# Kernel tuning notes

Hardware: AMD Instinct MI355X
Metric: run time of the kernel (lower is better)

## Reference

```python
import math
import jax, jax.numpy as jnp
import numpy as np

B, V, F, H, W = 1, 2, 4, 16, 28
TPF = H * W            # 448 tokens per frame
VS = F * TPF           # 1792 tokens per view
TS = V * VS            # 3584 total tokens
DIM, NH = 1536, 12
HD = DIM // NH         # 128
EPS = 1e-6
SCALE = 1.0 / math.sqrt(HD)


def _rope_angle_table(max_len=1024):
    # Wan-style 3D rope: head_dim//2 = 64 channels split [22, 21, 21] for (f, h, w)
    parts = []
    for full in (44, 42, 42):
        inv = 1.0 / (10000.0 ** (np.arange(0, full, 2) / full))
        parts.append(np.outer(np.arange(max_len), inv))
    return np.concatenate(parts, axis=1).astype(np.float32)  # [max_len, 64]


def setup_inputs():
    key = jax.random.key(0)
    ks = jax.random.split(key, 6)
    p = lambda k, shp: 0.02 * jax.random.normal(k, shp, dtype=jnp.float32)
    return {
        "x": jax.random.normal(ks[0], (B, TS, DIM), dtype=jnp.float32),
        "freqs": jnp.asarray(_rope_angle_table()),
        "q_w": p(ks[1], (DIM, DIM)), "q_b": jnp.zeros((DIM,), jnp.float32),
        "k_w": p(ks[2], (DIM, DIM)), "k_b": jnp.zeros((DIM,), jnp.float32),
        "v_w": p(ks[3], (DIM, DIM)), "v_b": jnp.zeros((DIM,), jnp.float32),
        "o_w": p(ks[4], (DIM, DIM)), "o_b": jnp.zeros((DIM,), jnp.float32),
        "norm_q_w": jnp.ones((DIM,), jnp.float32),
        "norm_k_w": jnp.ones((DIM,), jnp.float32),
        "seq_lens": jnp.full((B,), TS, jnp.int32),
        "view_grid_sizes": jnp.broadcast_to(jnp.array([F, H, W], jnp.int32), (B, V, 3)),
        "view_seq_lens": jnp.full((B, V), VS, jnp.int32),
        "total_seq_lens": jnp.full((B,), TS, jnp.int32),
    }


def _rms_norm(x, w):
    x32 = x.astype(jnp.float32)
    y = x32 * jax.lax.rsqrt(jnp.mean(x32 * x32, axis=-1, keepdims=True) + EPS)
    return y.astype(x.dtype) * w


def _rope_angles(freqs):
    c = HD // 2                                   # 64
    s0, s1 = c - 2 * (c // 3), c // 3             # 22, 21
    af = jnp.broadcast_to(freqs[:F, None, None, :s0], (F, H, W, s0))
    ah = jnp.broadcast_to(freqs[None, :H, None, s0:s0 + s1], (F, H, W, s1))
    aw = jnp.broadcast_to(freqs[None, None, :W, s0 + s1:c], (F, H, W, c - s0 - s1))
    return jnp.concatenate([af, ah, aw], axis=-1).reshape(VS, c)  # [VS, 64]


def _apply_rope(x, ang):
    # x: [N, S, NH, HD]; pairs are (x[..., 2i], x[..., 2i+1]) as in view_as_complex
    cos = jnp.cos(ang)[None, :, None, :]
    sin = jnp.sin(ang)[None, :, None, :]
    xr = x.reshape(x.shape[:-1] + (HD // 2, 2))
    r0 = xr[..., 0] * cos - xr[..., 1] * sin
    r1 = xr[..., 0] * sin + xr[..., 1] * cos
    return jnp.stack([r0, r1], axis=-1).reshape(x.shape)


def _attn_lse(q, k, v):
    # q,k,v: [N, S, NH, HD] -> out [N, S, NH, HD], lse [N, S, NH]
    logits = jnp.einsum('bqhd,bkhd->bhqk', q, k) * SCALE
    lse = jax.nn.logsumexp(logits, axis=-1)       # [N, NH, Sq]
    p = jnp.exp(logits - lse[..., None])
    out = jnp.einsum('bhqk,bkhd->bqhd', p, v)
    return out, jnp.transpose(lse, (0, 2, 1))


def _forward(x, freqs, q_w, q_b, k_w, k_b, v_w, v_b, o_w, o_b, norm_q_w, norm_k_w):
    xv = x[:, :TS]
    q = _rms_norm(xv @ q_w.T + q_b, norm_q_w)
    k = _rms_norm(xv @ k_w.T + k_b, norm_k_w)
    v = xv @ v_w.T + v_b
    q = q.reshape(B * V, VS, NH, HD)
    k = k.reshape(B * V, VS, NH, HD)
    v = v.reshape(B * V, VS, NH, HD)
    ang = _rope_angles(freqs)
    q = _apply_rope(q, ang)
    k = _apply_rope(k, ang)
    # intra-view attention over the full view sequence
    out_i, lse_i = _attn_lse(q, k, v)
    # cross-view per-frame attention: swap the two views for K/V
    k_sw = k.reshape(B, V, F, TPF, NH, HD)[:, ::-1].reshape(B * V * F, TPF, NH, HD)
    v_sw = v.reshape(B, V, F, TPF, NH, HD)[:, ::-1].reshape(B * V * F, TPF, NH, HD)
    q_c = q.reshape(B * V * F, TPF, NH, HD)
    out_c, lse_c = _attn_lse(q_c, k_sw, v_sw)
    out_i = out_i.reshape(B, V, F, TPF, NH, HD)
    lse_i = lse_i.reshape(B, V, F, TPF, NH)
    out_c = out_c.reshape(B, V, F, TPF, NH, HD)
    lse_c = lse_c.reshape(B, V, F, TPF, NH)
    # online-softmax-style LSE merge of the two attention results
    lse_u = jnp.logaddexp(lse_i, lse_c)
    fused = (jnp.exp(lse_i - lse_u)[..., None] * out_i
             + jnp.exp(lse_c - lse_u)[..., None] * out_c)
    fused = fused.reshape(B, TS, DIM)
    return fused @ o_w.T + o_b


def reference(x, freqs, q_w, q_b, k_w, k_b, v_w, v_b, o_w, o_b, norm_q_w, norm_k_w,
              seq_lens, view_grid_sizes, view_seq_lens, total_seq_lens):
    del seq_lens, view_grid_sizes, view_seq_lens, total_seq_lens  # validated layout constants
    return _forward(x, freqs, q_w, q_b, k_w, k_b, v_w, v_b, o_w, o_b, norm_q_w, norm_k_w)
```

## Files before the change

kernel.cpp:

```cpp
#include <hip/hip_runtime.h>

#define TS 3584
#define VS 1792
#define TPF 448
#define NHEAD 12
#define HDIM 128
#define DMODEL 1536
#define QK_PRESCALE (0.08838834764831845f * 1.4426950408889634f)

typedef unsigned short u16;
typedef unsigned int u32;
typedef __attribute__((ext_vector_type(8))) short bf16x8;
typedef __attribute__((ext_vector_type(4))) float f32x4;

__device__ __forceinline__ float u2f(u32 u) { union { u32 u; float f; } c; c.u = u; return c.f; }
__device__ __forceinline__ float blo(u32 u) { return u2f(u << 16); }
__device__ __forceinline__ float bhi(u32 u) { return u2f(u & 0xffff0000u); }
__device__ __forceinline__ u16 f2b(float f) {
  union { float f; u32 u; } c; c.f = f;
  return (u16)((c.u + 0x7fffu + ((c.u >> 16) & 1u)) >> 16);
}

__device__ __forceinline__ float exp2fast(float x) {
#if __has_builtin(__builtin_amdgcn_exp2f)
  return __builtin_amdgcn_exp2f(x);
#else
  float r; asm("v_exp_f32 %0, %1" : "=v"(r) : "v"(x)); return r;
#endif
}

__device__ __forceinline__ void gl16(const u16* g, u16* l) {
  __builtin_amdgcn_global_load_lds(
      (const __attribute__((address_space(1))) void*)g,
      (__attribute__((address_space(3))) void*)l, 16, 0, 0);
}

__global__ __launch_bounds__(256) void convert_bf16(
    const float* __restrict__ x, const float* __restrict__ qw,
    const float* __restrict__ kw, const float* __restrict__ vw,
    const float* __restrict__ ow, u16* __restrict__ xb,
    u16* __restrict__ wqkv, u16* __restrict__ owb) {
  const int z = blockIdx.y;
  const float* src;
  u16* dst;
  int n8;
  if (z == 0)      { src = x;  dst = xb;  n8 = TS * DMODEL / 8; }
  else if (z == 4) { src = ow; dst = owb; n8 = DMODEL * DMODEL / 8; }
  else {
    src = (z == 1) ? qw : (z == 2) ? kw : vw;
    dst = wqkv + (size_t)(z - 1) * DMODEL * DMODEL;
    n8 = DMODEL * DMODEL / 8;
  }
  const int idx = blockIdx.x * 256 + threadIdx.x;
  if (idx >= n8) return;
  const float4 a = ((const float4*)src)[2 * idx];
  const float4 b = ((const float4*)src)[2 * idx + 1];
  uint4 o;
  o.x = (u32)f2b(a.x) | ((u32)f2b(a.y) << 16);
  o.y = (u32)f2b(a.z) | ((u32)f2b(a.w) << 16);
  o.z = (u32)f2b(b.x) | ((u32)f2b(b.y) << 16);
  o.w = (u32)f2b(b.z) | ((u32)f2b(b.w) << 16);
  ((uint4*)dst)[idx] = o;
}

template <bool QKV>
__global__ __launch_bounds__(256) void gemm_mfma(
    const u16* __restrict__ A, const u16* __restrict__ W,
    const float* __restrict__ b0, const float* __restrict__ b1,
    const float* __restrict__ b2,
    u16* __restrict__ o0, u16* __restrict__ o1, u16* __restrict__ o2,
    float* __restrict__ of) {
  __shared__ __align__(16) u16 Als[128 * 64];
  __shared__ __align__(16) u16 Bls[128 * 64];
  const int t = threadIdx.x;
  const int wave = t >> 6, lane = t & 63, col = lane & 15, quad = lane >> 4;
  const int nwg = gridDim.x * gridDim.y;
  const int dlin = blockIdx.y * gridDim.x + blockIdx.x;
  const int wk = (dlin & 7) * (nwg >> 3) + (dlin >> 3);
  const int by = wk / gridDim.x, bx = wk - by * gridDim.x;
  const int m0 = by * 128, n0 = bx * 128;
  const int wm = (wave & 1) * 64, wn = (wave >> 1) * 64;

  const int srow = lane >> 3;
  const int sch = (lane & 7) ^ srow;
  const u16* pA[4];
  const u16* pB[4];
#pragma unroll
  for (int i = 0; i < 4; ++i) {
    const int r = i * 32 + wave * 8 + srow;
    pA[i] = A + (size_t)(m0 + r) * DMODEL + sch * 8;
    pB[i] = W + (size_t)(n0 + r) * DMODEL + sch * 8;
  }

  f32x4 acc[4][4];
#pragma unroll
  for (int i = 0; i < 4; ++i)
#pragma unroll
    for (int j = 0; j < 4; ++j) acc[i][j] = (f32x4){0.f, 0.f, 0.f, 0.f};

  for (int k0 = 0; k0 < DMODEL; k0 += 64) {
    __syncthreads();
#pragma unroll
    for (int i = 0; i < 4; ++i) {
      gl16(pA[i] + k0, &Als[i * 2048 + wave * 512]);
      gl16(pB[i] + k0, &Bls[i * 2048 + wave * 512]);
    }
    __syncthreads();
#pragma unroll
    for (int s = 0; s < 2; ++s) {
      bf16x8 af[4], bv[4];
#pragma unroll
      for (int i = 0; i < 4; ++i) {
        const int r = wm + i * 16 + col;
        af[i] = *(const bf16x8*)&Als[r * 64 + (((s * 4 + quad) ^ (r & 7)) * 8)];
      }
#pragma unroll
      for (int j = 0; j < 4; ++j) {
        const int r = wn + j * 16 + col;
        bv[j] = *(const bf16x8*)&Bls[r * 64 + (((s * 4 + quad) ^ (r & 7)) * 8)];
      }
#pragma unroll
      for (int i = 0; i < 4; ++i)
#pragma unroll
        for (int j = 0; j < 4; ++j)
          acc[i][j] = __builtin_amdgcn_mfma_f32_16x16x32_bf16(af[i], bv[j], acc[i][j], 0, 0, 0);
    }
  }

#pragma unroll
  for (int j = 0; j < 4; ++j) {
    const int ng = n0 + wn + j * 16 + col;
    if constexpr (QKV) {
      const int sec = ng / DMODEL;
      const int nn = ng - sec * DMODEL;
      u16* dst = sec == 0 ? o0 : (sec == 1 ? o1 : o2);
      const float bias = sec == 0 ? b0[nn] : (sec == 1 ? b1[nn] : b2[nn]);
#pragma unroll
      for (int i = 0; i < 4; ++i) {
        const int mb = m0 + wm + i * 16 + quad * 4;
#pragma unroll
        for (int r = 0; r < 4; ++r)
          dst[(size_t)(mb + r) * DMODEL + nn] = f2b(acc[i][j][r] + bias);
      }
    } else {
      const float bias = b0[ng];
#pragma unroll
      for (int i = 0; i < 4; ++i) {
        const int mb = m0 + wm + i * 16 + quad * 4;
#pragma unroll
        for (int r = 0; r < 4; ++r)
          of[(size_t)(mb + r) * DMODEL + ng] = acc[i][j][r] + bias;
      }
    }
  }
}

__global__ __launch_bounds__(256) void rmsnorm_rope(
    u16* qbuf, u16* kbuf, const float* __restrict__ freqs,
    const float* __restrict__ nqw, const float* __restrict__ nkw) {
  const int tok = blockIdx.x;
  u32* row = (u32*)((blockIdx.y == 0 ? qbuf : kbuf) + (size_t)tok * DMODEL);
  const float* w = blockIdx.y == 0 ? nqw : nkw;
  const int t = threadIdx.x;
  const u32 u0 = row[t], u1 = row[t + 256], u2 = row[t + 512];
  float px[3] = { blo(u0), blo(u1), blo(u2) };
  float py[3] = { bhi(u0), bhi(u1), bhi(u2) };
  float ss = px[0] * px[0] + py[0] * py[0] + px[1] * px[1] + py[1] * py[1] +
             px[2] * px[2] + py[2] * py[2];
#pragma unroll
  for (int off = 32; off; off >>= 1) ss += __shfl_xor(ss, off);
  __shared__ float red[4];
  if ((t & 63) == 0) red[t >> 6] = ss;
  __syncthreads();
  float rstd = rsqrtf((red[0] + red[1] + red[2] + red[3]) * (1.0f / DMODEL) + 1e-6f);
  if (blockIdx.y == 0) rstd *= QK_PRESCALE;
  const int p = tok % VS;
  const int fi = p / TPF, rem = p % TPF, hi = rem / 28, wi = rem % 28;
#pragma unroll
  for (int jj = 0; jj < 3; ++jj) {
    const int pj = t + jj * 256;
    const int i = pj & 63;
    const int prow = (i < 22) ? fi : ((i < 43) ? hi : wi);
    const float ang = freqs[prow * 64 + i];
    float sn, cs;
    sincosf(ang, &sn, &cs);
    const float a = px[jj] * rstd * w[2 * pj], b = py[jj] * rstd * w[2 * pj + 1];
    row[pj] = (u32)f2b(a * cs - b * sn) | ((u32)f2b(a * sn + b * cs) << 16);
  }
}

__global__ __launch_bounds__(128) void transpose_v(
    const u16* __restrict__ v, u16* __restrict__ vt) {
  __shared__ __align__(16) u16 T[128 * 128];
  const int h = blockIdx.y;
  const int t0 = blockIdx.x * 128;
  const int t = threadIdx.x;
#pragma unroll
  for (int i = 0; i < 16; ++i) {
    int idx = t + i * 128;
    int tok = idx >> 4, hd8 = idx & 15;
    *(uint4*)&T[tok * 128 + ((hd8 ^ (tok & 7)) * 8)] =
        *(const uint4*)(v + (size_t)(t0 + tok) * DMODEL + h * HDIM + hd8 * 8);
  }
  __syncthreads();
  const int hb = t >> 3;
#pragma unroll
  for (int half = 0; half < 2; ++half) {
    const int tb = (t & 7) + half * 8;
    uint4 M[8];
#pragma unroll
    for (int r = 0; r < 8; ++r)
      M[r] = *(const uint4*)&T[(tb * 8 + r) * 128 + ((hb ^ r) * 8)];
    uint4 O[8];
#pragma unroll
    for (int c2 = 0; c2 < 4; ++c2) {
      const u32* A = (const u32*)&M[2 * c2];
      const u32* Bp = (const u32*)&M[2 * c2 + 1];
#pragma unroll
      for (int jh = 0; jh < 4; ++jh) {
        u32 a = A[jh], b = Bp[jh];
        ((u32*)&O[2 * jh])[c2] = (a & 0xffffu) | (b << 16);
        ((u32*)&O[2 * jh + 1])[c2] = (a >> 16) | (b & 0xffff0000u);
      }
    }
#pragma unroll
    for (int j = 0; j < 8; ++j)
      *(uint4*)(vt + (size_t)(h * HDIM + hb * 8 + j) * TS + t0 + tb * 8) = O[j];
  }
}

__global__ __launch_bounds__(256) void attn_mfma(
    const u16* __restrict__ q, const u16* __restrict__ k,
    const u16* __restrict__ vt, u16* __restrict__ fused) {
  __shared__ __align__(16) u16 Kls[2 * 32 * 128];
  __shared__ __align__(16) u16 Vls[2 * 128 * 32];
  const int t = threadIdx.x;
  const int wave = t >> 6, lane = t & 63;
  const int col = lane & 15, quad = lane >> 4;
  const int d = blockIdx.y * 56 + blockIdx.x;
  const int wk = (d & 7) * 84 + (d >> 3);
  const int h = wk / 56;
  const int qb = wk - h * 56;
  const int q0 = qb * 64;
  const int vview = q0 / VS;
  const int fidx = (q0 % VS) / TPF;
  const int base0 = vview * VS;
  const int base1 = (1 - vview) * VS + fidx * TPF;
  const int jmpd = base1 - base0 - 1760;

  bf16x8 qfrag[4];
#pragma unroll
  for (int c = 0; c < 4; ++c)
    qfrag[c] = *(const bf16x8*)(q + (size_t)(q0 + wave * 16 + col) * DMODEL +
                                h * HDIM + ((c * 4 + quad) << 3));

  const u16* ksrc[2];
  const u16* vsrc[2];
#pragma unroll
  for (int j = 0; j < 2; ++j) {
    const int ci = (wave * 2 + j) * 64 + lane;
    const int key = ci >> 4, c = ci & 15;
    const int k4 = ((key >> 1) & 12) | (key & 3);
    ksrc[j] = k + (size_t)(base0 + key) * DMODEL + h * HDIM + ((c ^ k4) << 3);
    const int hd = ci >> 2, sl = ci & 3;
    vsrc[j] = vt + (size_t)(h * HDIM + hd) * TS + base0 + ((sl ^ (hd & 3)) << 3);
  }
  const int r0 = ((col & 12) << 1) | (col & 3);
  int koffu[4];
#pragma unroll
  for (int c = 0; c < 4; ++c) koffu[c] = r0 * 128 + (((c * 4 + quad) ^ col) << 3);
  const int voffu = col * 32 + ((quad ^ (col & 3)) << 3);

#pragma unroll
  for (int j = 0; j < 2; ++j) {
    gl16(ksrc[j], &Kls[(wave * 2 + j) * 512]);
    gl16(vsrc[j], &Vls[(wave * 2 + j) * 512]);
  }
  int ts = 1;
#pragma unroll
  for (int j = 0; j < 2; ++j) { ksrc[j] += 32 * DMODEL; vsrc[j] += 32; }

  f32x4 accO[8];
#pragma unroll
  for (int c = 0; c < 8; ++c) accO[c] = (f32x4){0.f, 0.f, 0.f, 0.f};
  float m_run = -1e30f, l_run = 0.f;

#define AITER(CUR, LAST)                                                       \
  do {                                                                         \
    if (!(LAST)) {                                                             \
      _Pragma("unroll") for (int j = 0; j < 2; ++j) {                          \
        gl16(ksrc[j], &Kls[((CUR) ^ 1) * 4096 + (wave * 2 + j) * 512]);        \
        gl16(vsrc[j], &Vls[((CUR) ^ 1) * 4096 + (wave * 2 + j) * 512]);        \
      }                                                                        \
      const int dd = (ts == 55) ? jmpd : 32; ++ts;                             \
      _Pragma("unroll") for (int j = 0; j < 2; ++j) {                          \
        ksrc[j] += (ptrdiff_t)dd * DMODEL; vsrc[j] += dd;                      \
      }                                                                        \
    }                                                                          \
    asm volatile("s_waitcnt vmcnt(%0)" ::"i"((LAST) ? 0 : 4) : "memory");      \
    __builtin_amdgcn_s_barrier();                                              \
    asm volatile("" ::: "memory");                                             \
    f32x4 s0 = (f32x4){0.f, 0.f, 0.f, 0.f}, s1 = s0;                           \
    __builtin_amdgcn_s_setprio(1);                                             \
    _Pragma("unroll") for (int c = 0; c < 4; ++c) {                            \
      bf16x8 ka0 = *(const bf16x8*)&Kls[(CUR) * 4096 + koffu[c]];              \
      bf16x8 ka1 = *(const bf16x8*)&Kls[(CUR) * 4096 + koffu[c] + 512];        \
      s0 = __builtin_amdgcn_mfma_f32_16x16x32_bf16(ka0, qfrag[c], s0, 0, 0, 0);\
      s1 = __builtin_amdgcn_mfma_f32_16x16x32_bf16(ka1, qfrag[c], s1, 0, 0, 0);\
    }                                                                          \
    __builtin_amdgcn_s_setprio(0);                                             \
    float lmax = fmaxf(fmaxf(fmaxf(s0[0], s0[1]), fmaxf(s0[2], s0[3])),        \
                       fmaxf(fmaxf(s1[0], s1[1]), fmaxf(s1[2], s1[3])));       \
    lmax = fmaxf(lmax, __shfl_xor(lmax, 16));                                  \
    lmax = fmaxf(lmax, __shfl_xor(lmax, 32));                                  \
    if (__any(lmax > m_run + 8.f)) {                                           \
      const float mnew = fmaxf(m_run, lmax);                                   \
      const float alpha = exp2fast(m_run - mnew);                              \
      _Pragma("unroll") for (int c = 0; c < 8; ++c) {                          \
        accO[c][0] *= alpha; accO[c][1] *= alpha;                              \
        accO[c][2] *= alpha; accO[c][3] *= alpha;                              \
      }                                                                        \
      l_run *= alpha;                                                          \
      m_run = mnew;                                                            \
    }                                                                          \
    float ps = 0.f;                                                            \
    _Pragma("unroll") for (int r = 0; r < 4; ++r) {                            \
      s0[r] = exp2fast(s0[r] - m_run); s1[r] = exp2fast(s1[r] - m_run);        \
      ps += s0[r] + s1[r];                                                     \
    }                                                                          \
    union { u32 w[4]; bf16x8 v; } pu;                                          \
    asm("v_cvt_pk_bf16_f32 %0, %1, %2" : "=v"(pu.w[0]) : "v"(s0[0]), "v"(s0[1])); \
    asm("v_cvt_pk_bf16_f32 %0, %1, %2" : "=v"(pu.w[1]) : "v"(s0[2]), "v"(s0[3])); \
    asm("v_cvt_pk_bf16_f32 %0, %1, %2" : "=v"(pu.w[2]) : "v"(s1[0]), "v"(s1[1])); \
    asm("v_cvt_pk_bf16_f32 %0, %1, %2" : "=v"(pu.w[3]) : "v"(s1[2]), "v"(s1[3])); \
    __builtin_amdgcn_s_setprio(1);                                             \
    _Pragma("unroll") for (int c = 0; c < 8; ++c) {                            \
      bf16x8 va = *(const bf16x8*)&Vls[(CUR) * 4096 + voffu + c * 512];        \
      accO[c] = __builtin_amdgcn_mfma_f32_16x16x32_bf16(va, pu.v, accO[c], 0, 0, 0); \
    }                                                                          \
    __builtin_amdgcn_s_setprio(0);                                             \
    if (!(LAST)) {                                                             \
      asm volatile("" ::: "memory");                                           \
      __builtin_amdgcn_s_barrier();                                            \
      asm volatile("" ::: "memory");                                           \
    }                                                                          \
    ps += __shfl_xor(ps, 16);                                                  \
    ps += __shfl_xor(ps, 32);                                                  \
    l_run += ps;                                                               \
  } while (0)

  for (int tt = 0; tt < 34; ++tt) {
    AITER(0, false);
    AITER(1, false);
  }
  AITER(0, false);
  AITER(1, true);
#undef AITER

  const float inv = 1.0f / l_run;
  const int token = q0 + wave * 16 + col;
  u16* orow = fused + (size_t)token * DMODEL + h * HDIM;
#pragma unroll
  for (int c = 0; c < 8; ++c) {
    uint2 ov;
    ov.x = (u32)f2b(accO[c][0] * inv) | ((u32)f2b(accO[c][1] * inv) << 16);
    ov.y = (u32)f2b(accO[c][2] * inv) | ((u32)f2b(accO[c][3] * inv) << 16);
    *(uint2*)(orow + c * 16 + quad * 4) = ov;
  }
}

extern "C" void kernel_launch(void* const* d_in, const int* in_sizes, int n_in,
                              void* d_out, int out_size, void* d_ws, size_t ws_size,
                              hipStream_t stream) {
  (void)in_sizes; (void)n_in; (void)out_size; (void)ws_size;
  const float* x   = (const float*)d_in[0];
  const float* fr  = (const float*)d_in[1];
  const float* qw  = (const float*)d_in[2];
  const float* qb  = (const float*)d_in[3];
  const float* kw  = (const float*)d_in[4];
  const float* kb  = (const float*)d_in[5];
  const float* vw  = (const float*)d_in[6];
  const float* vb  = (const float*)d_in[7];
  const float* ow  = (const float*)d_in[8];
  const float* ob  = (const float*)d_in[9];
  const float* nqw = (const float*)d_in[10];
  const float* nkw = (const float*)d_in[11];

  u16* qf   = (u16*)d_ws;
  u16* vf   = qf + (size_t)TS * DMODEL;
  u16* xb   = vf + (size_t)TS * DMODEL;
  u16* wqkv = xb + (size_t)TS * DMODEL;
  u16* owb  = wqkv + (size_t)3 * DMODEL * DMODEL;
  u16* kf   = (u16*)d_out;
  u16* vtb  = (u16*)d_out + (size_t)TS * DMODEL;

  convert_bf16<<<dim3(TS * DMODEL / 8 / 256, 5), dim3(256), 0, stream>>>(
      x, qw, kw, vw, ow, xb, wqkv, owb);
  gemm_mfma<true><<<dim3(3 * DMODEL / 128, TS / 128), dim3(256), 0, stream>>>(
      xb, wqkv, qb, kb, vb, qf, kf, vf, nullptr);
  rmsnorm_rope<<<dim3(TS, 2), dim3(256), 0, stream>>>(qf, kf, fr, nqw, nkw);
  transpose_v<<<dim3(TS / 128, NHEAD), dim3(128), 0, stream>>>(vf, vtb);
  attn_mfma<<<dim3(TS / 64, NHEAD), dim3(256), 0, stream>>>(qf, kf, vtb, qf);
  gemm_mfma<false><<<dim3(DMODEL / 128, TS / 128), dim3(256), 0, stream>>>(
      qf, owb, ob, nullptr, nullptr, nullptr, nullptr, nullptr, (float*)d_out);
}
```

Measured before the change: 321.6 us.

## Fuse V transpose into QKV GEMM epilogue and load V fragments directly

The QKV GEMM epilogue for the V section now transposes its tile through shared memory and writes V directly in head-dim-major layout, so the separate transpose_v kernel and its read-write pass over V are gone. The attention kernel drops the V shared-memory staging buffer and instead loads V MFMA fragments from global memory into registers, prefetched one iteration ahead. The wait counts are adjusted to match. This shortens the per-iteration LDS traffic and removes one launch, at the cost of more registers and relying on cache-friendly direct global loads for V.

```diff
diff --git a/kernel.cpp b/kernel.cpp
--- a/kernel.cpp
+++ b/kernel.cpp
@@ -10,6 +10,7 @@
 
 typedef unsigned short u16;
 typedef unsigned int u32;
+typedef unsigned long long u64;
 typedef __attribute__((ext_vector_type(8))) short bf16x8;
 typedef __attribute__((ext_vector_type(4))) float f32x4;
 
@@ -70,8 +71,9 @@
     const float* __restrict__ b2,
     u16* __restrict__ o0, u16* __restrict__ o1, u16* __restrict__ o2,
     float* __restrict__ of) {
-  __shared__ __align__(16) u16 Als[128 * 64];
-  __shared__ __align__(16) u16 Bls[128 * 64];
+  __shared__ __align__(16) u16 SH[128 * 128];
+  u16* const Als = SH;
+  u16* const Bls = SH + 128 * 64;
   const int t = threadIdx.x;
   const int wave = t >> 6, lane = t & 63, col = lane & 15, quad = lane >> 4;
   const int nwg = gridDim.x * gridDim.y;
@@ -127,14 +129,41 @@
     }
   }
 
-#pragma unroll
-  for (int j = 0; j < 4; ++j) {
-    const int ng = n0 + wn + j * 16 + col;
-    if constexpr (QKV) {
-      const int sec = ng / DMODEL;
-      const int nn = ng - sec * DMODEL;
-      u16* dst = sec == 0 ? o0 : (sec == 1 ? o1 : o2);
-      const float bias = sec == 0 ? b0[nn] : (sec == 1 ? b1[nn] : b2[nn]);
+  if constexpr (QKV) {
+    const int sec = n0 / DMODEL;
+    if (sec == 2) {
+      __syncthreads();
+#pragma unroll
+      for (int j = 0; j < 4; ++j) {
+        const int hdl = wn + j * 16 + col;
+        const float bias = b2[n0 - 2 * DMODEL + hdl];
+#pragma unroll
+        for (int i = 0; i < 4; ++i) {
+          const int tokl = wm + i * 16 + quad * 4;
+          u64 pk = (u64)f2b(acc[i][j][0] + bias) |
+                   ((u64)f2b(acc[i][j][1] + bias) << 16) |
+                   ((u64)f2b(acc[i][j][2] + bias) << 32) |
+                   ((u64)f2b(acc[i][j][3] + bias) << 48);
+          *(u64*)&SH[hdl * 128 + (((tokl >> 3) ^ (hdl & 15)) * 8) + (tokl & 7)] = pk;
+        }
+      }
+      __syncthreads();
+      const int hgl = (n0 - 2 * DMODEL) >> 7;
+#pragma unroll
+      for (int it = 0; it < 8; ++it) {
+        const int idx = t + it * 256;
+        const int row = idx >> 4, ch = idx & 15;
+        uint4 w = *(const uint4*)&SH[row * 128 + ((ch ^ (row & 15)) * 8)];
+        *(uint4*)(o2 + (size_t)(hgl * HDIM + row) * TS + m0 + ch * 8) = w;
+      }
+      return;
+    }
+    u16* dst = (sec == 0) ? o0 : o1;
+    const float* bp = (sec == 0) ? b0 : b1;
+#pragma unroll
+    for (int j = 0; j < 4; ++j) {
+      const int nn = n0 - sec * DMODEL + wn + j * 16 + col;
+      const float bias = bp[nn];
 #pragma unroll
       for (int i = 0; i < 4; ++i) {
         const int mb = m0 + wm + i * 16 + quad * 4;
@@ -142,7 +171,11 @@
         for (int r = 0; r < 4; ++r)
           dst[(size_t)(mb + r) * DMODEL + nn] = f2b(acc[i][j][r] + bias);
       }
-    } else {
+    }
+  } else {
+#pragma unroll
+    for (int j = 0; j < 4; ++j) {
+      const int ng = n0 + wn + j * 16 + col;
       const float bias = b0[ng];
 #pragma unroll
       for (int i = 0; i < 4; ++i) {
@@ -189,51 +222,10 @@
   }
 }
 
-__global__ __launch_bounds__(128) void transpose_v(
-    const u16* __restrict__ v, u16* __restrict__ vt) {
-  __shared__ __align__(16) u16 T[128 * 128];
-  const int h = blockIdx.y;
-  const int t0 = blockIdx.x * 128;
-  const int t = threadIdx.x;
-#pragma unroll
-  for (int i = 0; i < 16; ++i) {
-    int idx = t + i * 128;
-    int tok = idx >> 4, hd8 = idx & 15;
-    *(uint4*)&T[tok * 128 + ((hd8 ^ (tok & 7)) * 8)] =
-        *(const uint4*)(v + (size_t)(t0 + tok) * DMODEL + h * HDIM + hd8 * 8);
-  }
-  __syncthreads();
-  const int hb = t >> 3;
-#pragma unroll
-  for (int half = 0; half < 2; ++half) {
-    const int tb = (t & 7) + half * 8;
-    uint4 M[8];
-#pragma unroll
-    for (int r = 0; r < 8; ++r)
-      M[r] = *(const uint4*)&T[(tb * 8 + r) * 128 + ((hb ^ r) * 8)];
-    uint4 O[8];
-#pragma unroll
-    for (int c2 = 0; c2 < 4; ++c2) {
-      const u32* A = (const u32*)&M[2 * c2];
-      const u32* Bp = (const u32*)&M[2 * c2 + 1];
-#pragma unroll
-      for (int jh = 0; jh < 4; ++jh) {
-        u32 a = A[jh], b = Bp[jh];
-        ((u32*)&O[2 * jh])[c2] = (a & 0xffffu) | (b << 16);
-        ((u32*)&O[2 * jh + 1])[c2] = (a >> 16) | (b & 0xffff0000u);
-      }
-    }
-#pragma unroll
-    for (int j = 0; j < 8; ++j)
-      *(uint4*)(vt + (size_t)(h * HDIM + hb * 8 + j) * TS + t0 + tb * 8) = O[j];
-  }
-}
-
 __global__ __launch_bounds__(256) void attn_mfma(
     const u16* __restrict__ q, const u16* __restrict__ k,
     const u16* __restrict__ vt, u16* __restrict__ fused) {
   __shared__ __align__(16) u16 Kls[2 * 32 * 128];
-  __shared__ __align__(16) u16 Vls[2 * 128 * 32];
   const int t = threadIdx.x;
   const int wave = t >> 6, lane = t & 63;
   const int col = lane & 15, quad = lane >> 4;
@@ -253,32 +245,33 @@
   for (int c = 0; c < 4; ++c)
     qfrag[c] = *(const bf16x8*)(q + (size_t)(q0 + wave * 16 + col) * DMODEL +
                                 h * HDIM + ((c * 4 + quad) << 3));
+  asm volatile("" ::: "memory");
 
   const u16* ksrc[2];
-  const u16* vsrc[2];
 #pragma unroll
   for (int j = 0; j < 2; ++j) {
     const int ci = (wave * 2 + j) * 64 + lane;
     const int key = ci >> 4, c = ci & 15;
     const int k4 = ((key >> 1) & 12) | (key & 3);
     ksrc[j] = k + (size_t)(base0 + key) * DMODEL + h * HDIM + ((c ^ k4) << 3);
-    const int hd = ci >> 2, sl = ci & 3;
-    vsrc[j] = vt + (size_t)(h * HDIM + hd) * TS + base0 + ((sl ^ (hd & 3)) << 3);
   }
   const int r0 = ((col & 12) << 1) | (col & 3);
   int koffu[4];
 #pragma unroll
   for (int c = 0; c < 4; ++c) koffu[c] = r0 * 128 + (((c * 4 + quad) ^ col) << 3);
-  const int voffu = col * 32 + ((quad ^ (col & 3)) << 3);
-
-#pragma unroll
-  for (int j = 0; j < 2; ++j) {
+  const u16* vbase = vt + (size_t)(h * HDIM + col) * TS + quad * 8;
+
+#pragma unroll
+  for (int j = 0; j < 2; ++j)
     gl16(ksrc[j], &Kls[(wave * 2 + j) * 512]);
-    gl16(vsrc[j], &Vls[(wave * 2 + j) * 512]);
-  }
-  int ts = 1;
-#pragma unroll
-  for (int j = 0; j < 2; ++j) { ksrc[j] += 32 * DMODEL; vsrc[j] += 32; }
+  asm volatile("" ::: "memory");
+  bf16x8 vfrag[8];
+#pragma unroll
+  for (int c = 0; c < 8; ++c)
+    vfrag[c] = *(const bf16x8*)(vbase + (size_t)c * (16 * TS) + base0);
+  int ts = 1, tv = 1, kbn = base0 + 32;
+#pragma unroll
+  for (int j = 0; j < 2; ++j) ksrc[j] += 32 * DMODEL;
 
   f32x4 accO[8];
 #pragma unroll
@@ -288,16 +281,13 @@
 #define AITER(CUR, LAST)                                                       \
   do {                                                                         \
     if (!(LAST)) {                                                             \
-      _Pragma("unroll") for (int j = 0; j < 2; ++j) {                          \
+      _Pragma("unroll") for (int j = 0; j < 2; ++j)                            \
         gl16(ksrc[j], &Kls[((CUR) ^ 1) * 4096 + (wave * 2 + j) * 512]);        \
-        gl16(vsrc[j], &Vls[((CUR) ^ 1) * 4096 + (wave * 2 + j) * 512]);        \
-      }                                                                        \
       const int dd = (ts == 55) ? jmpd : 32; ++ts;                             \
-      _Pragma("unroll") for (int j = 0; j < 2; ++j) {                          \
-        ksrc[j] += (ptrdiff_t)dd * DMODEL; vsrc[j] += dd;                      \
-      }                                                                        \
-    }                                                                          \
-    asm volatile("s_waitcnt vmcnt(%0)" ::"i"((LAST) ? 0 : 4) : "memory");      \
+      _Pragma("unroll") for (int j = 0; j < 2; ++j)                            \
+        ksrc[j] += (ptrdiff_t)dd * DMODEL;                                     \
+    }                                                                          \
+    asm volatile("s_waitcnt vmcnt(%0)" ::"i"((LAST) ? 8 : 10) : "memory");     \
     __builtin_amdgcn_s_barrier();                                              \
     asm volatile("" ::: "memory");                                             \
     f32x4 s0 = (f32x4){0.f, 0.f, 0.f, 0.f}, s1 = s0;                           \
@@ -334,19 +324,22 @@
     asm("v_cvt_pk_bf16_f32 %0, %1, %2" : "=v"(pu.w[2]) : "v"(s1[0]), "v"(s1[1])); \
     asm("v_cvt_pk_bf16_f32 %0, %1, %2" : "=v"(pu.w[3]) : "v"(s1[2]), "v"(s1[3])); \
     __builtin_amdgcn_s_setprio(1);                                             \
-    _Pragma("unroll") for (int c = 0; c < 8; ++c) {                            \
-      bf16x8 va = *(const bf16x8*)&Vls[(CUR) * 4096 + voffu + c * 512];        \
-      accO[c] = __builtin_amdgcn_mfma_f32_16x16x32_bf16(va, pu.v, accO[c], 0, 0, 0); \
-    }                                                                          \
+    _Pragma("unroll") for (int c = 0; c < 8; ++c)                              \
+      accO[c] = __builtin_amdgcn_mfma_f32_16x16x32_bf16(vfrag[c], pu.v, accO[c], 0, 0, 0); \
     __builtin_amdgcn_s_setprio(0);                                             \
+    if (!(LAST)) {                                                             \
+      _Pragma("unroll") for (int c = 0; c < 8; ++c)                            \
+        vfrag[c] = *(const bf16x8*)(vbase + (size_t)c * (16 * TS) + kbn);      \
+      kbn += (tv == 55) ? jmpd : 32; ++tv;                                     \
+    }                                                                          \
+    ps += __shfl_xor(ps, 16);                                                  \
+    ps += __shfl_xor(ps, 32);                                                  \
+    l_run += ps;                                                               \
     if (!(LAST)) {                                                             \
       asm volatile("" ::: "memory");                                           \
       __builtin_amdgcn_s_barrier();                                            \
       asm volatile("" ::: "memory");                                           \
     }                                                                          \
-    ps += __shfl_xor(ps, 16);                                                  \
-    ps += __shfl_xor(ps, 32);                                                  \
-    l_run += ps;                                                               \
   } while (0)
 
   for (int tt = 0; tt < 34; ++tt) {
@@ -397,9 +390,8 @@
   convert_bf16<<<dim3(TS * DMODEL / 8 / 256, 5), dim3(256), 0, stream>>>(
       x, qw, kw, vw, ow, xb, wqkv, owb);
   gemm_mfma<true><<<dim3(3 * DMODEL / 128, TS / 128), dim3(256), 0, stream>>>(
-      xb, wqkv, qb, kb, vb, qf, kf, vf, nullptr);
+      xb, wqkv, qb, kb, vb, qf, kf, vtb, nullptr);
   rmsnorm_rope<<<dim3(TS, 2), dim3(256), 0, stream>>>(qf, kf, fr, nqw, nkw);
-  transpose_v<<<dim3(TS / 128, NHEAD), dim3(128), 0, stream>>>(vf, vtb);
   attn_mfma<<<dim3(TS / 64, NHEAD), dim3(256), 0, stream>>>(qf, kf, vtb, qf);
   gemm_mfma<false><<<dim3(DMODEL / 128, TS / 128), dim3(256), 0, stream>>>(
       qf, owb, ob, nullptr, nullptr, nullptr, nullptr, nullptr, (float*)d_out);
```

New measurement: 433.0 us. 1.35x slower.
